# Kernel tuning notes

Measured on AMD Instinct MI355X. Metric: run time of the kernel, lower is better.

## Reference

```python
import jax, jax.numpy as jnp
import numpy as np

N = 50000   # nodes
E = 600000  # edges (avg degree ~12)
R = 8       # num_relations = 2 * n_speakers**2, n_speakers=2
B = 32      # num_bases = args.batch_size
GD, H1, H2 = 128, 128, 128


def setup_inputs() -> dict:
    key = jax.random.key(0)
    ks = jax.random.split(key, 16)
    w = lambda k, shape: jax.random.normal(k, shape, jnp.float32) * 0.05
    return {
        "node_features": jax.random.normal(ks[0], (N, GD), jnp.float32),
        "edge_index": jax.random.randint(ks[1], (2, E), 0, N),
        "edge_norm": jax.random.uniform(ks[2], (E,), jnp.float32),
        "edge_type": jax.random.randint(ks[3], (E,), 0, R),
        "basis": w(ks[4], (B, GD, H1)),
        "comp": w(ks[5], (R, B)),
        "root": w(ks[6], (GD, H1)),
        "bias1": jnp.zeros((H1,), jnp.float32),
        "w_key": w(ks[7], (H1, H2)),
        "b_key": jnp.zeros((H2,), jnp.float32),
        "w_query": w(ks[8], (H1, H2)),
        "b_query": jnp.zeros((H2,), jnp.float32),
        "w_value": w(ks[9], (H1, H2)),
        "b_value": jnp.zeros((H2,), jnp.float32),
        "w_skip": w(ks[10], (H1, H2)),
        "b_skip": jnp.zeros((H2,), jnp.float32),
    }


def reference(node_features, edge_index, edge_norm, edge_type, basis, comp,
              root, bias1, w_key, b_key, w_query, b_query, w_value, b_value,
              w_skip, b_skip):
    n = node_features.shape[0]
    r = comp.shape[0]
    src, dst = edge_index[0], edge_index[1]

    # ---- RGCNConv (basis decomposition, per-relation mean aggregation) ----
    W = jnp.einsum('rb,bio->rio', comp, basis)            # [R, GD, H1]
    xW = jnp.einsum('ni,rio->rno', node_features, W)      # [R, N, H1]
    msg = xW[edge_type, src]                              # [E, H1]
    seg = edge_type * n + dst                             # combined (relation, dst) segment id
    agg = jax.ops.segment_sum(msg, seg, num_segments=r * n).reshape(r, n, -1)
    cnt = jax.ops.segment_sum(jnp.ones(msg.shape[0], jnp.float32), seg,
                              num_segments=r * n).reshape(r, n, 1)
    h = (agg / jnp.maximum(cnt, 1.0)).sum(0) + node_features @ root + bias1

    # ---- ResGatedGraphConv: sigmoid(k_i + q_j) * v_j, sum-aggregated + skip ----
    k = h @ w_key + b_key
    q = h @ w_query + b_query
    v = h @ w_value + b_value
    m = jax.nn.sigmoid(k[dst] + q[src]) * v[src]          # [E, H2]
    out = jax.ops.segment_sum(m, dst, num_segments=n) + h @ w_skip + b_skip
    return out
```

## Files before the change

### kernel.cpp

```cpp
#include <hip/hip_runtime.h>
#include <stdint.h>

#define GD 128
#define H1 128
#define H2 128
#define NBASES 32
#define NREL 8
#define K1 (NREL*GD + GD)

typedef __attribute__((ext_vector_type(8))) short bf16x8;
typedef __attribute__((ext_vector_type(4))) float f32x4;

static inline size_t align256(size_t x){ return (x + 255) & ~(size_t)255; }

__device__ __forceinline__ float bf2f(uint32_t u16){
  union { uint32_t u; float f; } c; c.u = (u16 & 0xffffu) << 16; return c.f;
}
__device__ __forceinline__ unsigned short f2bf(float f){
  union { float f; uint32_t u; } c; c.f = f;
  uint32_t u = c.u;
  u += 0x7fffu + ((u >> 16) & 1u);
  return (unsigned short)(u >> 16);
}
__device__ __forceinline__ uint32_t pkbf(float a, float b){
  union { float f; uint32_t u; } ca, cb; ca.f = a; cb.f = b;
  return __builtin_amdgcn_perm(cb.u + 0x8000u, ca.u + 0x8000u, 0x07060302u);
}

__device__ __forceinline__ void async_copy16(void* lds_dst, const void* gsrc){
  __builtin_amdgcn_global_load_lds(
      (const __attribute__((address_space(1))) uint32_t*)gsrc,
      (__attribute__((address_space(3))) uint32_t*)lds_dst, 16, 0, 0);
}

__global__ void k_prep(const float* __restrict__ comp, const float* __restrict__ basis,
                       const float* __restrict__ root, unsigned short* __restrict__ B1t,
                       const float* __restrict__ wk, const float* __restrict__ wq,
                       const float* __restrict__ wv, const float* __restrict__ wsk,
                       const float* __restrict__ bk, const float* __restrict__ bq,
                       const float* __restrict__ bv, const float* __restrict__ bs,
                       unsigned short* __restrict__ B2t, float* __restrict__ Bb,
                       const float4* __restrict__ x, uint2* __restrict__ xout, int cnt4,
                       int4* __restrict__ cntz, int nz4){
  int b = blockIdx.x, t = threadIdx.x;
  if (b < 576){
    int idx = b*256 + t;
    int nn = idx / K1, kk = idx % K1;
    float v;
    if (kk < NREL*GD){
      int r = kk >> 7, i = kk & 127;
      float acc = 0.f;
      #pragma unroll
      for (int bb = 0; bb < NBASES; ++bb)
        acc += comp[r*NBASES + bb] * basis[((size_t)bb*GD + i)*H1 + nn];
      v = acc;
    } else {
      v = root[(size_t)(kk - NREL*GD)*H1 + nn];
    }
    B1t[idx] = f2bf(v);
  } else if (b < 576 + 256){
    int idx = (b - 576)*256 + t;
    int c = idx / H1, k = idx % H1;
    const float* w = (c < 128) ? wk : (c < 256) ? wq : (c < 384) ? wv : wsk;
    B2t[idx] = f2bf(w[(size_t)k*H2 + (c & 127)]);
    if (idx < 512){
      const float* bia = (idx < 128) ? bk : (idx < 256) ? bq : (idx < 384) ? bv : bs;
      Bb[idx] = bia[idx & 127];
    }
  } else {
    int cb = b - (576 + 256);
    int ncastb = (cnt4 + 255) >> 8;
    if (cb < ncastb){
      int i = cb*256 + t;
      if (i < cnt4){
        float4 v = x[i];
        uint2 o; o.x = pkbf(v.x, v.y); o.y = pkbf(v.z, v.w);
        xout[i] = o;
      }
    } else {
      int i = (cb - ncastb)*256 + t;
      if (i < nz4) cntz[i] = (int4){0,0,0,0};
    }
  }
}

__global__ void k_hist_rd(const int* __restrict__ dst, const int* __restrict__ typ,
                          int* __restrict__ cnt, int E, int n){
  int e = blockIdx.x*blockDim.x + threadIdx.x;
  if (e < E) atomicAdd(&cnt[typ[e]*n + dst[e]], 1);
}

__global__ void k_scanA(const int* __restrict__ deg, int* __restrict__ off,
                        int* __restrict__ btot, int len){
  __shared__ int wsum[16];
  int t = threadIdx.x, lane = t & 63, w = t >> 6;
  int i0 = blockIdx.x*8192 + t*8;
  int v[8];
  if (i0 + 7 < len){
    int4 va = *(const int4*)(deg + i0);
    int4 vb = *(const int4*)(deg + i0 + 4);
    v[0]=va.x; v[1]=va.y; v[2]=va.z; v[3]=va.w;
    v[4]=vb.x; v[5]=vb.y; v[6]=vb.z; v[7]=vb.w;
  } else {
    #pragma unroll
    for (int u = 0; u < 8; ++u) v[u] = (i0+u < len) ? deg[i0+u] : 0;
  }
  int s[8]; s[0] = v[0];
  #pragma unroll
  for (int u = 1; u < 8; ++u) s[u] = s[u-1] + v[u];
  int x = s[7];
  #pragma unroll
  for (int d = 1; d < 64; d <<= 1){
    int u = __shfl_up(x, d, 64);
    if (lane >= d) x += u;
  }
  if (lane == 63) wsum[w] = x;
  __syncthreads();
  if (t < 16){
    int y = wsum[t];
    #pragma unroll
    for (int d = 1; d < 16; d <<= 1){
      int u = __shfl_up(y, d, 16);
      if (t >= d) y += u;
    }
    wsum[t] = y;
  }
  __syncthreads();
  int woff = (w > 0) ? wsum[w-1] : 0;
  int excl = woff + x - s[7];
  #pragma unroll
  for (int u = 0; u < 8; ++u)
    if (i0+u < len) off[i0+u] = excl + s[u] - v[u];
  if (t == 0) btot[blockIdx.x] = wsum[15];
}

__global__ void k_scanB(const int* __restrict__ btot, int* __restrict__ off,
                        int* __restrict__ cursor, int len, int sentinel){
  int t = threadIdx.x, bid = blockIdx.x;
  int add = 0;
  for (int j = 0; j < bid; ++j) add += btot[j];
  int i0 = bid*8192 + t*8;
  #pragma unroll
  for (int u = 0; u < 8; ++u){
    int i = i0 + u;
    if (i < len){ int val = off[i] + add; off[i] = val; cursor[i] = val; }
  }
  if (bid == 0 && t == 0) off[len] = sentinel;
}

__global__ void k_scatter_rd(const int* __restrict__ src, const int* __restrict__ dst,
                             const int* __restrict__ typ, int* __restrict__ cursor,
                             int* __restrict__ pk, int E, int n){
  int e = blockIdx.x*blockDim.x + threadIdx.x;
  if (e >= E) return;
  int pos = atomicAdd(&cursor[typ[e]*n + dst[e]], 1);
  pk[pos] = src[e];
}

__global__ void k_edge1(const int* __restrict__ off_rd, const int* __restrict__ pk_rd,
                        const unsigned short* __restrict__ xbf,
                        unsigned short* __restrict__ Abig, int n, int npad){
  int wid = blockIdx.x*(blockDim.x >> 6) + (threadIdx.x >> 6);
  int lane = threadIdx.x & 63;
  if (wid >= npad) return;
  uint32_t* Arow = (uint32_t*)(Abig + (size_t)wid*K1);
  if (wid >= n){
    #pragma unroll
    for (int r = 0; r < 9; ++r) __builtin_nontemporal_store(0u, Arow + r*64 + lane);
    return;
  }
  const uint32_t* x32 = (const uint32_t*)xbf;
  int r8 = lane & 7;
  int o_r = off_rd[(size_t)r8*n + wid];
  int e_r = off_rd[(size_t)r8*n + wid + 1];
  int c_r = e_r - o_r;
  int c0_ = __builtin_amdgcn_readlane(c_r, 0), c1_ = __builtin_amdgcn_readlane(c_r, 1);
  int c2_ = __builtin_amdgcn_readlane(c_r, 2), c3_ = __builtin_amdgcn_readlane(c_r, 3);
  int c4_ = __builtin_amdgcn_readlane(c_r, 4), c5_ = __builtin_amdgcn_readlane(c_r, 5);
  int c6_ = __builtin_amdgcn_readlane(c_r, 6), c7_ = __builtin_amdgcn_readlane(c_r, 7);
  int o0_ = __builtin_amdgcn_readlane(o_r, 0), o1_ = __builtin_amdgcn_readlane(o_r, 1);
  int o2_ = __builtin_amdgcn_readlane(o_r, 2), o3_ = __builtin_amdgcn_readlane(o_r, 3);
  int o4_ = __builtin_amdgcn_readlane(o_r, 4), o5_ = __builtin_amdgcn_readlane(o_r, 5);
  int o6_ = __builtin_amdgcn_readlane(o_r, 6), o7_ = __builtin_amdgcn_readlane(o_r, 7);
  int p1 = c0_, p2 = p1 + c1_, p3 = p2 + c2_, p4 = p3 + c3_;
  int p5 = p4 + c4_, p6 = p5 + c5_, p7 = p6 + c6_, dg = p7 + c7_;

  float a0[8], a1[8];
  #pragma unroll
  for (int r = 0; r < 8; ++r){ a0[r] = 0.f; a1[r] = 0.f; }

  for (int jb = 0; jb < dg; jb += 64){
    int i = jb + lane;
    int adj = o0_, rel = 0;
    adj = (i >= p1) ? (o1_ - p1) : adj;  rel += (i >= p1);
    adj = (i >= p2) ? (o2_ - p2) : adj;  rel += (i >= p2);
    adj = (i >= p3) ? (o3_ - p3) : adj;  rel += (i >= p3);
    adj = (i >= p4) ? (o4_ - p4) : adj;  rel += (i >= p4);
    adj = (i >= p5) ? (o5_ - p5) : adj;  rel += (i >= p5);
    adj = (i >= p6) ? (o6_ - p6) : adj;  rel += (i >= p6);
    adj = (i >= p7) ? (o7_ - p7) : adj;  rel += (i >= p7);
    int m = dg - jb; if (m > 64) m = 64;
    int pj = (lane < m) ? pk_rd[adj + i] : 0;
    int jj = 0;
    for (; jj + 8 <= m; jj += 8){
      uint32_t g[8]; int rr[8];
      #pragma unroll
      for (int k = 0; k < 8; ++k){
        int s = __builtin_amdgcn_readlane(pj, jj + k);
        rr[k] = __builtin_amdgcn_readlane(rel, jj + k);
        g[k] = x32[(size_t)s*64 + lane];
      }
      #pragma unroll
      for (int k = 0; k < 8; ++k){
        float x0 = bf2f(g[k]), x1 = bf2f(g[k] >> 16);
        switch (rr[k]){
          case 0: a0[0]+=x0; a1[0]+=x1; break;
          case 1: a0[1]+=x0; a1[1]+=x1; break;
          case 2: a0[2]+=x0; a1[2]+=x1; break;
          case 3: a0[3]+=x0; a1[3]+=x1; break;
          case 4: a0[4]+=x0; a1[4]+=x1; break;
          case 5: a0[5]+=x0; a1[5]+=x1; break;
          case 6: a0[6]+=x0; a1[6]+=x1; break;
          default: a0[7]+=x0; a1[7]+=x1; break;
        }
      }
    }
    for (; jj < m; ++jj){
      int s = __builtin_amdgcn_readlane(pj, jj);
      int rk = __builtin_amdgcn_readlane(rel, jj);
      uint32_t gg = x32[(size_t)s*64 + lane];
      float x0 = bf2f(gg), x1 = bf2f(gg >> 16);
      switch (rk){
        case 0: a0[0]+=x0; a1[0]+=x1; break;
        case 1: a0[1]+=x0; a1[1]+=x1; break;
        case 2: a0[2]+=x0; a1[2]+=x1; break;
        case 3: a0[3]+=x0; a1[3]+=x1; break;
        case 4: a0[4]+=x0; a1[4]+=x1; break;
        case 5: a0[5]+=x0; a1[5]+=x1; break;
        case 6: a0[6]+=x0; a1[6]+=x1; break;
        default: a0[7]+=x0; a1[7]+=x1; break;
      }
    }
  }
  int cc[8] = {c0_, c1_, c2_, c3_, c4_, c5_, c6_, c7_};
  #pragma unroll
  for (int r = 0; r < 8; ++r){
    float inv = (cc[r] > 0) ? 1.f/(float)cc[r] : 0.f;
    __builtin_nontemporal_store(pkbf(a0[r]*inv, a1[r]*inv), Arow + r*64 + lane);
  }
  __builtin_nontemporal_store(x32[(size_t)wid*64 + lane], Arow + 512 + lane);
}

__launch_bounds__(256)
__global__ void k_gemm1(const unsigned short* __restrict__ A, const unsigned short* __restrict__ Bt,
                        const float* __restrict__ bias, unsigned short* __restrict__ h){
  __shared__ char lds[16384];
  int t = threadIdx.x, lane = t & 63, wave = t >> 6;
  int row0 = blockIdx.x * 128;
  int mrow = lane & 15, quad = lane >> 4;
  int wrow = (wave & 1) * 64, wcol = (wave >> 1) * 64;
  int s = (mrow >> 1) & 3;

  const unsigned short* Asrc = A + (size_t)(row0 + (t >> 2))*K1 + (((t & 3) ^ ((t >> 3) & 3)) << 3);
  const unsigned short* Bsrc = Bt + (size_t)(t >> 2)*K1 + (((t & 3) ^ ((t >> 3) & 3)) << 3);
  char* ldsw = lds + wave*1024;

  int aoff = (wrow + mrow)*64 + ((quad ^ s) << 4);
  int boff = 8192 + (wcol + mrow)*64 + ((quad ^ s) << 4);

  f32x4 acc[4][4];
  #pragma unroll
  for (int i = 0; i < 4; ++i)
    #pragma unroll
    for (int j = 0; j < 4; ++j) acc[i][j] = (f32x4){0.f,0.f,0.f,0.f};

  for (int kt = 0; kt < K1; kt += 32){
    __syncthreads();
    async_copy16(ldsw,         Asrc + kt);
    async_copy16(ldsw + 4096,  Asrc + (size_t)64*K1 + kt);
    async_copy16(ldsw + 8192,  Bsrc + kt);
    async_copy16(ldsw + 12288, Bsrc + (size_t)64*K1 + kt);
    __syncthreads();
    bf16x8 af[4], bf[4];
    #pragma unroll
    for (int i = 0; i < 4; ++i) af[i] = *(const bf16x8*)(lds + aoff + i*1024);
    #pragma unroll
    for (int j = 0; j < 4; ++j) bf[j] = *(const bf16x8*)(lds + boff + j*1024);
    #pragma unroll
    for (int i = 0; i < 4; ++i)
      #pragma unroll
      for (int j = 0; j < 4; ++j)
        acc[i][j] = __builtin_amdgcn_mfma_f32_16x16x32_bf16(af[i], bf[j], acc[i][j], 0, 0, 0);
  }
  #pragma unroll
  for (int j = 0; j < 4; ++j){
    int col = wcol + j*16 + mrow;
    float bcol = bias[col];
    #pragma unroll
    for (int i = 0; i < 4; ++i)
      #pragma unroll
      for (int rg = 0; rg < 4; ++rg){
        int row = wrow + i*16 + quad*4 + rg;
        h[(size_t)(row0 + row)*H1 + col] = f2bf(acc[i][j][rg] + bcol);
      }
  }
}

__launch_bounds__(256)
__global__ void k_gemm2(const unsigned short* __restrict__ A, const unsigned short* __restrict__ Bt,
                        const float* __restrict__ Bb, unsigned short* __restrict__ kqv,
                        unsigned short* __restrict__ skipb, int n){
  __shared__ char lds[16384];
  int t = threadIdx.x, lane = t & 63, wave = t >> 6;
  int row0 = blockIdx.x * 128;
  int c0 = blockIdx.y * 128;
  int mrow = lane & 15, quad = lane >> 4;
  int wrow = (wave & 1) * 64, wcol = (wave >> 1) * 64;
  int s = (mrow >> 1) & 3;

  const unsigned short* Asrc = A + (size_t)(row0 + (t >> 2))*H1 + (((t & 3) ^ ((t >> 3) & 3)) << 3);
  const unsigned short* Bsrc = Bt + (size_t)(c0 + (t >> 2))*H1 + (((t & 3) ^ ((t >> 3) & 3)) << 3);
  char* ldsw = lds + wave*1024;

  int aoff = (wrow + mrow)*64 + ((quad ^ s) << 4);
  int boff = 8192 + (wcol + mrow)*64 + ((quad ^ s) << 4);

  f32x4 acc[4][4];
  #pragma unroll
  for (int i = 0; i < 4; ++i)
    #pragma unroll
    for (int j = 0; j < 4; ++j) acc[i][j] = (f32x4){0.f,0.f,0.f,0.f};

  #pragma unroll
  for (int kt = 0; kt < H1; kt += 32){
    __syncthreads();
    async_copy16(ldsw,         Asrc + kt);
    async_copy16(ldsw + 4096,  Asrc + (size_t)64*H1 + kt);
    async_copy16(ldsw + 8192,  Bsrc + kt);
    async_copy16(ldsw + 12288, Bsrc + (size_t)64*H1 + kt);
    __syncthreads();
    bf16x8 af[4], bf[4];
    #pragma unroll
    for (int i = 0; i < 4; ++i) af[i] = *(const bf16x8*)(lds + aoff + i*1024);
    #pragma unroll
    for (int j = 0; j < 4; ++j) bf[j] = *(const bf16x8*)(lds + boff + j*1024);
    #pragma unroll
    for (int i = 0; i < 4; ++i)
      #pragma unroll
      for (int j = 0; j < 4; ++j)
        acc[i][j] = __builtin_amdgcn_mfma_f32_16x16x32_bf16(af[i], bf[j], acc[i][j], 0, 0, 0);
  }
  #pragma unroll
  for (int j = 0; j < 4; ++j){
    int col = c0 + wcol + j*16 + mrow;
    float bcol = Bb[col];
    #pragma unroll
    for (int i = 0; i < 4; ++i)
      #pragma unroll
// ... 14 lines not shown
        }
      }
  }
}

__global__ void k_edge2(const int* __restrict__ off_rd, const int* __restrict__ pk_rd,
                        const unsigned short* __restrict__ kqv,
                        const unsigned short* __restrict__ skipb,
                        float* __restrict__ out, int n){
  int wid = blockIdx.x*(blockDim.x >> 6) + (threadIdx.x >> 6);
  int lane = threadIdx.x & 63;
  if (wid >= n) return;
  const uint32_t* kv32 = (const uint32_t*)kqv;
  int r = lane & 7;
  int o_r = off_rd[(size_t)r*n + wid];
  int e_r = off_rd[(size_t)r*n + wid + 1];
  int c_r = e_r - o_r;
  int c0_ = __builtin_amdgcn_readlane(c_r, 0), c1_ = __builtin_amdgcn_readlane(c_r, 1);
  int c2_ = __builtin_amdgcn_readlane(c_r, 2), c3_ = __builtin_amdgcn_readlane(c_r, 3);
  int c4_ = __builtin_amdgcn_readlane(c_r, 4), c5_ = __builtin_amdgcn_readlane(c_r, 5);
  int c6_ = __builtin_amdgcn_readlane(c_r, 6), c7_ = __builtin_amdgcn_readlane(c_r, 7);
  int o0_ = __builtin_amdgcn_readlane(o_r, 0), o1_ = __builtin_amdgcn_readlane(o_r, 1);
  int o2_ = __builtin_amdgcn_readlane(o_r, 2), o3_ = __builtin_amdgcn_readlane(o_r, 3);
  int o4_ = __builtin_amdgcn_readlane(o_r, 4), o5_ = __builtin_amdgcn_readlane(o_r, 5);
  int o6_ = __builtin_amdgcn_readlane(o_r, 6), o7_ = __builtin_amdgcn_readlane(o_r, 7);
  int p1 = c0_, p2 = p1 + c1_, p3 = p2 + c2_, p4 = p3 + c3_;
  int p5 = p4 + c4_, p6 = p5 + c5_, p7 = p6 + c6_, dg = p7 + c7_;

  uint32_t ku = kv32[(size_t)wid*192 + lane];
  float k0 = bf2f(ku), k1 = bf2f(ku >> 16);
  float a0 = 0.f, a1 = 0.f;
  for (int jb = 0; jb < dg; jb += 64){
    int i = jb + lane;
    int adj = o0_;
    adj = (i >= p1) ? (o1_ - p1) : adj;
    adj = (i >= p2) ? (o2_ - p2) : adj;
    adj = (i >= p3) ? (o3_ - p3) : adj;
    adj = (i >= p4) ? (o4_ - p4) : adj;
    adj = (i >= p5) ? (o5_ - p5) : adj;
    adj = (i >= p6) ? (o6_ - p6) : adj;
    adj = (i >= p7) ? (o7_ - p7) : adj;
    int m = dg - jb; if (m > 64) m = 64;
    int pj = (lane < m) ? pk_rd[adj + i] : 0;
    int jj = 0;
    for (; jj + 8 <= m; jj += 8){
      uint2 q[8];
      #pragma unroll
      for (int k = 0; k < 8; ++k){
        int s = __builtin_amdgcn_readlane(pj, jj + k);
        q[k] = *(const uint2*)(kv32 + (size_t)s*192 + 64 + lane*2);
      }
      #pragma unroll
      for (int k = 0; k < 8; ++k){
        float qq0 = bf2f(q[k].x), qq1 = bf2f(q[k].x >> 16);
        float vv0 = bf2f(q[k].y), vv1 = bf2f(q[k].y >> 16);
        float g0 = 1.f / (1.f + __expf(-(k0 + qq0)));
        float g1 = 1.f / (1.f + __expf(-(k1 + qq1)));
        a0 += g0*vv0; a1 += g1*vv1;
      }
    }
    for (; jj < m; ++jj){
      int s = __builtin_amdgcn_readlane(pj, jj);
      uint2 qc = *(const uint2*)(kv32 + (size_t)s*192 + 64 + lane*2);
      float qq0 = bf2f(qc.x), qq1 = bf2f(qc.x >> 16);
      float vv0 = bf2f(qc.y), vv1 = bf2f(qc.y >> 16);
      float g0 = 1.f / (1.f + __expf(-(k0 + qq0)));
      float g1 = 1.f / (1.f + __expf(-(k1 + qq1)));
      a0 += g0*vv0; a1 += g1*vv1;
    }
  }
  uint32_t sk = ((const uint32_t*)skipb)[(size_t)wid*64 + lane];
  float2 cur; cur.x = a0 + bf2f(sk); cur.y = a1 + bf2f(sk >> 16);
  ((float2*)(out + (size_t)wid*H2))[lane] = cur;
}

extern "C" void kernel_launch(void* const* d_in, const int* in_sizes, int n_in,
                              void* d_out, int out_size, void* d_ws, size_t ws_size,
                              hipStream_t stream){
  const float* x     = (const float*)d_in[0];
  const int*   eidx  = (const int*)  d_in[1];
  const int*   etype = (const int*)  d_in[3];
  const float* basis = (const float*)d_in[4];
  const float* comp  = (const float*)d_in[5];
  const float* root  = (const float*)d_in[6];
  const float* bias1 = (const float*)d_in[7];
  const float* wk    = (const float*)d_in[8];
  const float* bk    = (const float*)d_in[9];
  const float* wq    = (const float*)d_in[10];
  const float* bq    = (const float*)d_in[11];
  const float* wv    = (const float*)d_in[12];
  const float* bv    = (const float*)d_in[13];
  const float* wsk   = (const float*)d_in[14];
  const float* bs    = (const float*)d_in[15];
  const int n = in_sizes[0] / GD;
  const int E = in_sizes[3];
  const int npad = (n + 127) & ~127;
  const int* esrc = eidx;
  const int* edst = eidx + E;
  float* out = (float*)d_out;

  char* w = (char*)d_ws;
  size_t off = 0;
  unsigned short* xbf  = (unsigned short*)(w + off); off = align256(off + (size_t)n*GD*2);
  unsigned short* Abig = (unsigned short*)(w + off); off = align256(off + (size_t)npad*K1*2);
  unsigned short* B1t  = (unsigned short*)(w + off); off = align256(off + (size_t)H1*K1*2);
  unsigned short* B2t  = (unsigned short*)(w + off); off = align256(off + (size_t)512*H1*2);
  float* Bb            = (float*)(w + off);          off = align256(off + 512*4);
  unsigned short* hbuf = (unsigned short*)(w + off); off = align256(off + (size_t)npad*H1*2);
  unsigned short* kqv  = (unsigned short*)(w + off); off = align256(off + (size_t)n*384*2);
  unsigned short* skipb= (unsigned short*)(w + off); off = align256(off + (size_t)npad*H2*2);
  int* cnt_rd          = (int*)(w + off);            off = align256(off + (size_t)(8*n+4)*4);
  int* off_rd          = (int*)(w + off);            off = align256(off + (size_t)(8*n+1)*4);
  int* cur_rd          = (int*)(w + off);            off = align256(off + (size_t)8*n*4);
  int* btot_rd         = (int*)(w + off);            off = align256(off + 64*4);
  int* pk_rd           = (int*)(w + off);            off = align256(off + (size_t)E*4);

  const int nblk_rd = (8*n + 8191) / 8192;
  const int cnt4 = n*GD/4;
  const int nz4  = (8*n + 3)/4;
  const int ncastb = (cnt4 + 255)/256;
  const int nzerob = (nz4 + 255)/256;

  k_prep<<<576 + 256 + ncastb + nzerob, 256, 0, stream>>>(
      comp, basis, root, B1t, wk, wq, wv, wsk, bk, bq, bv, bs, B2t, Bb,
      (const float4*)x, (uint2*)xbf, cnt4, (int4*)cnt_rd, nz4);
  k_hist_rd<<<(E + 255)/256, 256, 0, stream>>>(edst, etype, cnt_rd, E, n);
  k_scanA<<<nblk_rd, 1024, 0, stream>>>(cnt_rd, off_rd, btot_rd, 8*n);
  k_scanB<<<nblk_rd, 1024, 0, stream>>>(btot_rd, off_rd, cur_rd, 8*n, E);
  k_scatter_rd<<<(E + 255)/256, 256, 0, stream>>>(esrc, edst, etype, cur_rd, pk_rd, E, n);
  k_edge1<<<(npad + 3)/4, 256, 0, stream>>>(off_rd, pk_rd, xbf, Abig, n, npad);
  k_gemm1<<<npad/128, 256, 0, stream>>>(Abig, B1t, bias1, hbuf);
  k_gemm2<<<dim3(npad/128, 4), 256, 0, stream>>>(hbuf, B2t, Bb, kqv, skipb, n);
  k_edge2<<<(n + 3)/4, 256, 0, stream>>>(off_rd, pk_rd, kqv, skipb, out, n);
}
```

Measured before the change: 390.8 us.

## Transform per-relation features before aggregation and fuse bias and root into the edge gather

Reorders the relational conv. Each node's features are first multiplied by all eight relation weights plus root in one GEMM, giving a wide Z buffer. Edge aggregation then gathers rows of Z with per-edge 1/count weights and adds root and bias, so the large concatenated A matrix and its K=1152 GEMM go away. The histogram is also folded into the prep kernel and the count buffer is cleared with a memset. The cost of this is that the gather now reads slices of a much larger buffer (about 115MB) instead of the compact bf16 features, which may hurt cache locality.

Measured after the change: 380.6 us. 1.03x faster.

```diff
diff --git a/kernel.cpp b/kernel.cpp
--- a/kernel.cpp
+++ b/kernel.cpp
@@ -6,7 +6,7 @@
 #define H2 128
 #define NBASES 32
 #define NREL 8
-#define K1 (NREL*GD + GD)
+#define KZ 1152
 
 typedef __attribute__((ext_vector_type(8))) short bf16x8;
 typedef __attribute__((ext_vector_type(4))) float f32x4;
@@ -34,30 +34,32 @@
 }
 
 __global__ void k_prep(const float* __restrict__ comp, const float* __restrict__ basis,
-                       const float* __restrict__ root, unsigned short* __restrict__ B1t,
+                       const float* __restrict__ root, unsigned short* __restrict__ Bz,
                        const float* __restrict__ wk, const float* __restrict__ wq,
                        const float* __restrict__ wv, const float* __restrict__ wsk,
                        const float* __restrict__ bk, const float* __restrict__ bq,
                        const float* __restrict__ bv, const float* __restrict__ bs,
                        unsigned short* __restrict__ B2t, float* __restrict__ Bb,
                        const float4* __restrict__ x, uint2* __restrict__ xout, int cnt4,
-                       int4* __restrict__ cntz, int nz4){
+                       uint32_t* __restrict__ xpadz, int npadz,
+                       const int* __restrict__ edst, const int* __restrict__ etyp,
+                       int* __restrict__ cnt, int E, int n){
   int b = blockIdx.x, t = threadIdx.x;
   if (b < 576){
     int idx = b*256 + t;
-    int nn = idx / K1, kk = idx % K1;
+    int row = idx >> 7, i = idx & 127;
+    int r = row >> 7, o = row & 127;
     float v;
-    if (kk < NREL*GD){
-      int r = kk >> 7, i = kk & 127;
+    if (r < 8){
       float acc = 0.f;
       #pragma unroll
       for (int bb = 0; bb < NBASES; ++bb)
-        acc += comp[r*NBASES + bb] * basis[((size_t)bb*GD + i)*H1 + nn];
+        acc += comp[r*NBASES + bb] * basis[((size_t)bb*GD + i)*H1 + o];
       v = acc;
     } else {
-      v = root[(size_t)(kk - NREL*GD)*H1 + nn];
-    }
-    B1t[idx] = f2bf(v);
+      v = root[(size_t)i*H1 + o];
+    }
+    Bz[idx] = f2bf(v);
   } else if (b < 576 + 256){
     int idx = (b - 576)*256 + t;
     int c = idx / H1, k = idx % H1;
@@ -77,17 +79,14 @@
         uint2 o; o.x = pkbf(v.x, v.y); o.y = pkbf(v.z, v.w);
         xout[i] = o;
       }
+    } else if (cb < ncastb + 12){
+      int i = (cb - ncastb)*256 + t;
+      if (i < npadz) xpadz[i] = 0u;
     } else {
-      int i = (cb - ncastb)*256 + t;
-      if (i < nz4) cntz[i] = (int4){0,0,0,0};
-    }
-  }
-}
-
-__global__ void k_hist_rd(const int* __restrict__ dst, const int* __restrict__ typ,
-                          int* __restrict__ cnt, int E, int n){
-  int e = blockIdx.x*blockDim.x + threadIdx.x;
-  if (e < E) atomicAdd(&cnt[typ[e]*n + dst[e]], 1);
+      int e = (cb - ncastb - 12)*256 + t;
+      if (e < E) atomicAdd(&cnt[etyp[e]*n + edst[e]], 1);
+    }
+  }
 }
 
 __global__ void k_scanA(const int* __restrict__ deg, int* __restrict__ off,
@@ -157,23 +156,77 @@
   pk[pos] = src[e];
 }
 
+__launch_bounds__(256)
+__global__ void k_zgemm(const unsigned short* __restrict__ A, const unsigned short* __restrict__ Bt,
+                        unsigned short* __restrict__ Z){
+  __shared__ char lds[16384];
+  int t = threadIdx.x, lane = t & 63, wave = t >> 6;
+  int row0 = blockIdx.x * 128;
+  int c0 = blockIdx.y * 128;
+  int mrow = lane & 15, quad = lane >> 4;
+  int wrow = (wave & 1) * 64, wcol = (wave >> 1) * 64;
+  int s = (mrow >> 1) & 3;
+
+  const unsigned short* Asrc = A + (size_t)(row0 + (t >> 2))*H1 + (((t & 3) ^ ((t >> 3) & 3)) << 3);
+  const unsigned short* Bsrc = Bt + (size_t)(c0 + (t >> 2))*H1 + (((t & 3) ^ ((t >> 3) & 3)) << 3);
+  char* ldsw = lds + wave*1024;
+
+  int aoff = (wrow + mrow)*64 + ((quad ^ s) << 4);
+  int boff = 8192 + (wcol + mrow)*64 + ((quad ^ s) << 4);
+
+  f32x4 acc[4][4];
+  #pragma unroll
+  for (int i = 0; i < 4; ++i)
+    #pragma unroll
+    for (int j = 0; j < 4; ++j) acc[i][j] = (f32x4){0.f,0.f,0.f,0.f};
+
+  #pragma unroll
+  for (int kt = 0; kt < H1; kt += 32){
+    __syncthreads();
+    async_copy16(ldsw,         Asrc + kt);
+    async_copy16(ldsw + 4096,  Asrc + (size_t)64*H1 + kt);
+    async_copy16(ldsw + 8192,  Bsrc + kt);
+    async_copy16(ldsw + 12288, Bsrc + (size_t)64*H1 + kt);
+    __syncthreads();
+    bf16x8 af[4], bf[4];
+    #pragma unroll
+    for (int i = 0; i < 4; ++i) af[i] = *(const bf16x8*)(lds + aoff + i*1024);
+    #pragma unroll
+    for (int j = 0; j < 4; ++j) bf[j] = *(const bf16x8*)(lds + boff + j*1024);
+    #pragma unroll
+    for (int i = 0; i < 4; ++i)
+      #pragma unroll
+      for (int j = 0; j < 4; ++j)
+        acc[i][j] = __builtin_amdgcn_mfma_f32_16x16x32_bf16(af[i], bf[j], acc[i][j], 0, 0, 0);
+  }
+  #pragma unroll
+  for (int j = 0; j < 4; ++j){
+    int col = c0 + wcol + j*16 + mrow;
+    #pragma unroll
+    for (int i = 0; i < 4; ++i)
+      #pragma unroll
+      for (int rg = 0; rg < 4; ++rg){
+        int row = row0 + wrow + i*16 + quad*4 + rg;
+        Z[(size_t)row*KZ + col] = f2bf(acc[i][j][rg]);
+      }
+  }
+}
+
 __global__ void k_edge1(const int* __restrict__ off_rd, const int* __restrict__ pk_rd,
-                        const unsigned short* __restrict__ xbf,
-                        unsigned short* __restrict__ Abig, int n, int npad){
+                        const unsigned short* __restrict__ Zb,
+                        const float* __restrict__ bias1,
+                        unsigned short* __restrict__ h, int n, int npad){
   int wid = blockIdx.x*(blockDim.x >> 6) + (threadIdx.x >> 6);
   int lane = threadIdx.x & 63;
   if (wid >= npad) return;
-  uint32_t* Arow = (uint32_t*)(Abig + (size_t)wid*K1);
-  if (wid >= n){
-    #pragma unroll
-    for (int r = 0; r < 9; ++r) __builtin_nontemporal_store(0u, Arow + r*64 + lane);
-    return;
-  }
-  const uint32_t* x32 = (const uint32_t*)xbf;
+  uint32_t* hrow = (uint32_t*)(h + (size_t)wid*H1);
+  if (wid >= n){ hrow[lane] = 0u; return; }
+  const uint32_t* Z32 = (const uint32_t*)Zb;
   int r8 = lane & 7;
   int o_r = off_rd[(size_t)r8*n + wid];
   int e_r = off_rd[(size_t)r8*n + wid + 1];
   int c_r = e_r - o_r;
+  float ic_r = (c_r > 0) ? (1.f/(float)c_r) : 0.f;
   int c0_ = __builtin_amdgcn_readlane(c_r, 0), c1_ = __builtin_amdgcn_readlane(c_r, 1);
   int c2_ = __builtin_amdgcn_readlane(c_r, 2), c3_ = __builtin_amdgcn_readlane(c_r, 3);
   int c4_ = __builtin_amdgcn_readlane(c_r, 4), c5_ = __builtin_amdgcn_readlane(c_r, 5);
@@ -182,128 +235,58 @@
   int o2_ = __builtin_amdgcn_readlane(o_r, 2), o3_ = __builtin_amdgcn_readlane(o_r, 3);
   int o4_ = __builtin_amdgcn_readlane(o_r, 4), o5_ = __builtin_amdgcn_readlane(o_r, 5);
   int o6_ = __builtin_amdgcn_readlane(o_r, 6), o7_ = __builtin_amdgcn_readlane(o_r, 7);
+  float i0f = __int_as_float(__builtin_amdgcn_readlane(__float_as_int(ic_r), 0));
+  float i1f = __int_as_float(__builtin_amdgcn_readlane(__float_as_int(ic_r), 1));
+  float i2f = __int_as_float(__builtin_amdgcn_readlane(__float_as_int(ic_r), 2));
+  float i3f = __int_as_float(__builtin_amdgcn_readlane(__float_as_int(ic_r), 3));
+  float i4f = __int_as_float(__builtin_amdgcn_readlane(__float_as_int(ic_r), 4));
+  float i5f = __int_as_float(__builtin_amdgcn_readlane(__float_as_int(ic_r), 5));
+  float i6f = __int_as_float(__builtin_amdgcn_readlane(__float_as_int(ic_r), 6));
+  float i7f = __int_as_float(__builtin_amdgcn_readlane(__float_as_int(ic_r), 7));
   int p1 = c0_, p2 = p1 + c1_, p3 = p2 + c2_, p4 = p3 + c3_;
   int p5 = p4 + c4_, p6 = p5 + c5_, p7 = p6 + c6_, dg = p7 + c7_;
 
-  float a0[8], a1[8];
-  #pragma unroll
-  for (int r = 0; r < 8; ++r){ a0[r] = 0.f; a1[r] = 0.f; }
-
+  float a0 = 0.f, a1 = 0.f;
   for (int jb = 0; jb < dg; jb += 64){
     int i = jb + lane;
     int adj = o0_, rel = 0;
-    adj = (i >= p1) ? (o1_ - p1) : adj;  rel += (i >= p1);
-    adj = (i >= p2) ? (o2_ - p2) : adj;  rel += (i >= p2);
-    adj = (i >= p3) ? (o3_ - p3) : adj;  rel += (i >= p3);
-    adj = (i >= p4) ? (o4_ - p4) : adj;  rel += (i >= p4);
-    adj = (i >= p5) ? (o5_ - p5) : adj;  rel += (i >= p5);
-    adj = (i >= p6) ? (o6_ - p6) : adj;  rel += (i >= p6);
-    adj = (i >= p7) ? (o7_ - p7) : adj;  rel += (i >= p7);
+    float wv = i0f;
+    adj = (i >= p1) ? (o1_ - p1) : adj;  rel += (i >= p1);  wv = (i >= p1) ? i1f : wv;
+    adj = (i >= p2) ? (o2_ - p2) : adj;  rel += (i >= p2);  wv = (i >= p2) ? i2f : wv;
+    adj = (i >= p3) ? (o3_ - p3) : adj;  rel += (i >= p3);  wv = (i >= p3) ? i3f : wv;
+    adj = (i >= p4) ? (o4_ - p4) : adj;  rel += (i >= p4);  wv = (i >= p4) ? i4f : wv;
+    adj = (i >= p5) ? (o5_ - p5) : adj;  rel += (i >= p5);  wv = (i >= p5) ? i5f : wv;
+    adj = (i >= p6) ? (o6_ - p6) : adj;  rel += (i >= p6);  wv = (i >= p6) ? i6f : wv;
+    adj = (i >= p7) ? (o7_ - p7) : adj;  rel += (i >= p7);  wv = (i >= p7) ? i7f : wv;
     int m = dg - jb; if (m > 64) m = 64;
     int pj = (lane < m) ? pk_rd[adj + i] : 0;
+    int gidx = pj*(KZ/2) + rel*64;
     int jj = 0;
     for (; jj + 8 <= m; jj += 8){
-      uint32_t g[8]; int rr[8];
+      uint32_t g[8]; float wgt[8];
       #pragma unroll
       for (int k = 0; k < 8; ++k){
-        int s = __builtin_amdgcn_readlane(pj, jj + k);
-        rr[k] = __builtin_amdgcn_readlane(rel, jj + k);
-        g[k] = x32[(size_t)s*64 + lane];
+        int gx = __builtin_amdgcn_readlane(gidx, jj + k);
+        wgt[k] = __int_as_float(__builtin_amdgcn_readlane(__float_as_int(wv), jj + k));
+        g[k] = Z32[(size_t)(uint32_t)gx + lane];
       }
       #pragma unroll
       for (int k = 0; k < 8; ++k){
-        float x0 = bf2f(g[k]), x1 = bf2f(g[k] >> 16);
-        switch (rr[k]){
-          case 0: a0[0]+=x0; a1[0]+=x1; break;
-          case 1: a0[1]+=x0; a1[1]+=x1; break;
-          case 2: a0[2]+=x0; a1[2]+=x1; break;
-          case 3: a0[3]+=x0; a1[3]+=x1; break;
-          case 4: a0[4]+=x0; a1[4]+=x1; break;
-          case 5: a0[5]+=x0; a1[5]+=x1; break;
-          case 6: a0[6]+=x0; a1[6]+=x1; break;
-          default: a0[7]+=x0; a1[7]+=x1; break;
-        }
+        a0 += bf2f(g[k]) * wgt[k];
+        a1 += bf2f(g[k] >> 16) * wgt[k];
       }
     }
     for (; jj < m; ++jj){
-      int s = __builtin_amdgcn_readlane(pj, jj);
-      int rk = __builtin_amdgcn_readlane(rel, jj);
-      uint32_t gg = x32[(size_t)s*64 + lane];
-      float x0 = bf2f(gg), x1 = bf2f(gg >> 16);
-      switch (rk){
-        case 0: a0[0]+=x0; a1[0]+=x1; break;
-        case 1: a0[1]+=x0; a1[1]+=x1; break;
-        case 2: a0[2]+=x0; a1[2]+=x1; break;
-        case 3: a0[3]+=x0; a1[3]+=x1; break;
-        case 4: a0[4]+=x0; a1[4]+=x1; break;
-        case 5: a0[5]+=x0; a1[5]+=x1; break;
-        case 6: a0[6]+=x0; a1[6]+=x1; break;
-        default: a0[7]+=x0; a1[7]+=x1; break;
-      }
-    }
-  }
-  int cc[8] = {c0_, c1_, c2_, c3_, c4_, c5_, c6_, c7_};
-  #pragma unroll
-  for (int r = 0; r < 8; ++r){
-    float inv = (cc[r] > 0) ? 1.f/(float)cc[r] : 0.f;
-    __builtin_nontemporal_store(pkbf(a0[r]*inv, a1[r]*inv), Arow + r*64 + lane);
-  }
-  __builtin_nontemporal_store(x32[(size_t)wid*64 + lane], Arow + 512 + lane);
-}
-
-__launch_bounds__(256)
-__global__ void k_gemm1(const unsigned short* __restrict__ A, const unsigned short* __restrict__ Bt,
-                        const float* __restrict__ bias, unsigned short* __restrict__ h){
-  __shared__ char lds[16384];
-  int t = threadIdx.x, lane = t & 63, wave = t >> 6;
-  int row0 = blockIdx.x * 128;
-  int mrow = lane & 15, quad = lane >> 4;
-  int wrow = (wave & 1) * 64, wcol = (wave >> 1) * 64;
-  int s = (mrow >> 1) & 3;
-
-  const unsigned short* Asrc = A + (size_t)(row0 + (t >> 2))*K1 + (((t & 3) ^ ((t >> 3) & 3)) << 3);
-  const unsigned short* Bsrc = Bt + (size_t)(t >> 2)*K1 + (((t & 3) ^ ((t >> 3) & 3)) << 3);
-  char* ldsw = lds + wave*1024;
-
-  int aoff = (wrow + mrow)*64 + ((quad ^ s) << 4);
-  int boff = 8192 + (wcol + mrow)*64 + ((quad ^ s) << 4);
-
-  f32x4 acc[4][4];
-  #pragma unroll
-  for (int i = 0; i < 4; ++i)
-    #pragma unroll
-    for (int j = 0; j < 4; ++j) acc[i][j] = (f32x4){0.f,0.f,0.f,0.f};
-
-  for (int kt = 0; kt < K1; kt += 32){
-    __syncthreads();
-    async_copy16(ldsw,         Asrc + kt);
-    async_copy16(ldsw + 4096,  Asrc + (size_t)64*K1 + kt);
-    async_copy16(ldsw + 8192,  Bsrc + kt);
-    async_copy16(ldsw + 12288, Bsrc + (size_t)64*K1 + kt);
-    __syncthreads();
-    bf16x8 af[4], bf[4];
-    #pragma unroll
-    for (int i = 0; i < 4; ++i) af[i] = *(const bf16x8*)(lds + aoff + i*1024);
-    #pragma unroll
-    for (int j = 0; j < 4; ++j) bf[j] = *(const bf16x8*)(lds + boff + j*1024);
-    #pragma unroll
-    for (int i = 0; i < 4; ++i)
-      #pragma unroll
-      for (int j = 0; j < 4; ++j)
-        acc[i][j] = __builtin_amdgcn_mfma_f32_16x16x32_bf16(af[i], bf[j], acc[i][j], 0, 0, 0);
-  }
-  #pragma unroll
-  for (int j = 0; j < 4; ++j){
-    int col = wcol + j*16 + mrow;
-    float bcol = bias[col];
-    #pragma unroll
-    for (int i = 0; i < 4; ++i)
-      #pragma unroll
-      for (int rg = 0; rg < 4; ++rg){
-        int row = wrow + i*16 + quad*4 + rg;
-        h[(size_t)(row0 + row)*H1 + col] = f2bf(acc[i][j][rg] + bcol);
-      }
-  }
+      int gx = __builtin_amdgcn_readlane(gidx, jj);
+      float wg = __int_as_float(__builtin_amdgcn_readlane(__float_as_int(wv), jj));
+      uint32_t gg = Z32[(size_t)(uint32_t)gx + lane];
+      a0 += bf2f(gg) * wg;
+      a1 += bf2f(gg >> 16) * wg;
+    }
+  }
+  uint32_t zr = Z32[(size_t)wid*(KZ/2) + 512 + lane];
+  float2 bb = ((const float2*)bias1)[lane];
+  hrow[lane] = pkbf(a0 + bf2f(zr) + bb.x, a1 + bf2f(zr >> 16) + bb.y);
 }
 
 __launch_bounds__(256)
@@ -473,9 +456,9 @@
 
   char* w = (char*)d_ws;
   size_t off = 0;
-  unsigned short* xbf  = (unsigned short*)(w + off); off = align256(off + (size_t)n*GD*2);
-  unsigned short* Abig = (unsigned short*)(w + off); off = align256(off + (size_t)npad*K1*2);
-  unsigned short* B1t  = (unsigned short*)(w + off); off = align256(off + (size_t)H1*K1*2);
+  unsigned short* xbf  = (unsigned short*)(w + off); off = align256(off + (size_t)npad*GD*2);
+  unsigned short* Zbuf = (unsigned short*)(w + off); off = align256(off + (size_t)npad*KZ*2);
+  unsigned short* Bz   = (unsigned short*)(w + off); off = align256(off + (size_t)KZ*H1*2);
   unsigned short* B2t  = (unsigned short*)(w + off); off = align256(off + (size_t)512*H1*2);
   float* Bb            = (float*)(w + off);          off = align256(off + 512*4);
   unsigned short* hbuf = (unsigned short*)(w + off); off = align256(off + (size_t)npad*H1*2);
@@ -489,19 +472,22 @@
 
   const int nblk_rd = (8*n + 8191) / 8192;
   const int cnt4 = n*GD/4;
-  const int nz4  = (8*n + 3)/4;
   const int ncastb = (cnt4 + 255)/256;
-  const int nzerob = (nz4 + 255)/256;
-
-  k_prep<<<576 + 256 + ncastb + nzerob, 256, 0, stream>>>(
-      comp, basis, root, B1t, wk, wq, wv, wsk, bk, bq, bv, bs, B2t, Bb,
-      (const float4*)x, (uint2*)xbf, cnt4, (int4*)cnt_rd, nz4);
-  k_hist_rd<<<(E + 255)/256, 256, 0, stream>>>(edst, etype, cnt_rd, E, n);
+  const int histb  = (E + 255)/256;
+  const int npadz  = (npad - n)*GD/2;
+
+  hipMemsetAsync(cnt_rd, 0, (size_t)8*n*4, stream);
+
+  k_prep<<<576 + 256 + ncastb + 12 + histb, 256, 0, stream>>>(
+      comp, basis, root, Bz, wk, wq, wv, wsk, bk, bq, bv, bs, B2t, Bb,
+      (const float4*)x, (uint2*)xbf, cnt4,
+      (uint32_t*)(xbf + (size_t)n*GD), npadz,
+      edst, etype, cnt_rd, E, n);
   k_scanA<<<nblk_rd, 1024, 0, stream>>>(cnt_rd, off_rd, btot_rd, 8*n);
   k_scanB<<<nblk_rd, 1024, 0, stream>>>(btot_rd, off_rd, cur_rd, 8*n, E);
   k_scatter_rd<<<(E + 255)/256, 256, 0, stream>>>(esrc, edst, etype, cur_rd, pk_rd, E, n);
-  k_edge1<<<(npad + 3)/4, 256, 0, stream>>>(off_rd, pk_rd, xbf, Abig, n, npad);
-  k_gemm1<<<npad/128, 256, 0, stream>>>(Abig, B1t, bias1, hbuf);
+  k_zgemm<<<dim3(npad/128, KZ/128), 256, 0, stream>>>(xbf, Bz, Zbuf);
+  k_edge1<<<(npad + 3)/4, 256, 0, stream>>>(off_rd, pk_rd, Zbuf, bias1, hbuf, n, npad);
   k_gemm2<<<dim3(npad/128, 4), 256, 0, stream>>>(hbuf, B2t, Bb, kqv, skipb, n);
   k_edge2<<<(n + 3)/4, 256, 0, stream>>>(off_rd, pk_rd, kqv, skipb, out, n);
 }
```

## Fuse relation aggregation with first GEMM via LDS tile, merge histogram into prep

Applied to the files above, without the earlier changes.

Replaces the edge1 gather kernel and the separate gemm1 with a single kernel that aggregates 32 nodes' per-relation means into a shared-memory A tile and multiplies it by the weight matrix with MFMA. This removes the round trip through the large Abig intermediate in global memory. The histogram atomics are folded into the prep kernel, with the counter zeroing done by a memset. A 4-edge unrolled tail is also added to both edge loops. The trade-off is that each block now holds about 74KB of LDS and reads B1t straight from global, which lowers occupancy. There is also an ordering risk: the histogram atomics run in the same launch as prep, so they depend on the memset finishing first.

New measurement: 403.2 us. 3.2% more time.

```diff
diff --git a/kernel.cpp b/kernel.cpp
--- a/kernel.cpp
+++ b/kernel.cpp
@@ -7,6 +7,7 @@
 #define NBASES 32
 #define NREL 8
 #define K1 (NREL*GD + GD)
+#define AROW 580
 
 typedef __attribute__((ext_vector_type(8))) short bf16x8;
 typedef __attribute__((ext_vector_type(4))) float f32x4;
@@ -25,12 +26,6 @@
 __device__ __forceinline__ uint32_t pkbf(float a, float b){
   union { float f; uint32_t u; } ca, cb; ca.f = a; cb.f = b;
   return __builtin_amdgcn_perm(cb.u + 0x8000u, ca.u + 0x8000u, 0x07060302u);
-}
-
-__device__ __forceinline__ void async_copy16(void* lds_dst, const void* gsrc){
-  __builtin_amdgcn_global_load_lds(
-      (const __attribute__((address_space(1))) uint32_t*)gsrc,
-      (__attribute__((address_space(3))) uint32_t*)lds_dst, 16, 0, 0);
 }
 
 __global__ void k_prep(const float* __restrict__ comp, const float* __restrict__ basis,
@@ -41,7 +36,8 @@
                        const float* __restrict__ bv, const float* __restrict__ bs,
                        unsigned short* __restrict__ B2t, float* __restrict__ Bb,
                        const float4* __restrict__ x, uint2* __restrict__ xout, int cnt4,
-                       int4* __restrict__ cntz, int nz4){
+                       const int* __restrict__ edst, const int* __restrict__ etyp,
+                       int* __restrict__ cnt, int E, int n){
   int b = blockIdx.x, t = threadIdx.x;
   if (b < 576){
     int idx = b*256 + t;
@@ -78,16 +74,10 @@
         xout[i] = o;
       }
     } else {
-      int i = (cb - ncastb)*256 + t;
-      if (i < nz4) cntz[i] = (int4){0,0,0,0};
-    }
-  }
-}
-
-__global__ void k_hist_rd(const int* __restrict__ dst, const int* __restrict__ typ,
-                          int* __restrict__ cnt, int E, int n){
-  int e = blockIdx.x*blockDim.x + threadIdx.x;
-  if (e < E) atomicAdd(&cnt[typ[e]*n + dst[e]], 1);
+      int e = (cb - ncastb)*256 + t;
+      if (e < E) atomicAdd(&cnt[etyp[e]*n + edst[e]], 1);
+    }
+  }
 }
 
 __global__ void k_scanA(const int* __restrict__ deg, int* __restrict__ off,
@@ -157,63 +147,110 @@
   pk[pos] = src[e];
 }
 
-__global__ void k_edge1(const int* __restrict__ off_rd, const int* __restrict__ pk_rd,
-                        const unsigned short* __restrict__ xbf,
-                        unsigned short* __restrict__ Abig, int n, int npad){
-  int wid = blockIdx.x*(blockDim.x >> 6) + (threadIdx.x >> 6);
-  int lane = threadIdx.x & 63;
-  if (wid >= npad) return;
-  uint32_t* Arow = (uint32_t*)(Abig + (size_t)wid*K1);
-  if (wid >= n){
-    #pragma unroll
-    for (int r = 0; r < 9; ++r) __builtin_nontemporal_store(0u, Arow + r*64 + lane);
-    return;
-  }
+__launch_bounds__(512)
+__global__ void k_fused1(const int* __restrict__ off_rd, const int* __restrict__ pk_rd,
+                         const unsigned short* __restrict__ xbf,
+                         const unsigned short* __restrict__ B1t,
+                         const float* __restrict__ bias1,
+                         unsigned short* __restrict__ h, int n){
+  __shared__ uint32_t Atile[32*AROW];
   const uint32_t* x32 = (const uint32_t*)xbf;
-  int r8 = lane & 7;
-  int o_r = off_rd[(size_t)r8*n + wid];
-  int e_r = off_rd[(size_t)r8*n + wid + 1];
-  int c_r = e_r - o_r;
-  int c0_ = __builtin_amdgcn_readlane(c_r, 0), c1_ = __builtin_amdgcn_readlane(c_r, 1);
-  int c2_ = __builtin_amdgcn_readlane(c_r, 2), c3_ = __builtin_amdgcn_readlane(c_r, 3);
-  int c4_ = __builtin_amdgcn_readlane(c_r, 4), c5_ = __builtin_amdgcn_readlane(c_r, 5);
-  int c6_ = __builtin_amdgcn_readlane(c_r, 6), c7_ = __builtin_amdgcn_readlane(c_r, 7);
-  int o0_ = __builtin_amdgcn_readlane(o_r, 0), o1_ = __builtin_amdgcn_readlane(o_r, 1);
-  int o2_ = __builtin_amdgcn_readlane(o_r, 2), o3_ = __builtin_amdgcn_readlane(o_r, 3);
-  int o4_ = __builtin_amdgcn_readlane(o_r, 4), o5_ = __builtin_amdgcn_readlane(o_r, 5);
-  int o6_ = __builtin_amdgcn_readlane(o_r, 6), o7_ = __builtin_amdgcn_readlane(o_r, 7);
-  int p1 = c0_, p2 = p1 + c1_, p3 = p2 + c2_, p4 = p3 + c3_;
-  int p5 = p4 + c4_, p6 = p5 + c5_, p7 = p6 + c6_, dg = p7 + c7_;
-
-  float a0[8], a1[8];
-  #pragma unroll
-  for (int r = 0; r < 8; ++r){ a0[r] = 0.f; a1[r] = 0.f; }
-
-  for (int jb = 0; jb < dg; jb += 64){
-    int i = jb + lane;
-    int adj = o0_, rel = 0;
-    adj = (i >= p1) ? (o1_ - p1) : adj;  rel += (i >= p1);
-    adj = (i >= p2) ? (o2_ - p2) : adj;  rel += (i >= p2);
-    adj = (i >= p3) ? (o3_ - p3) : adj;  rel += (i >= p3);
-    adj = (i >= p4) ? (o4_ - p4) : adj;  rel += (i >= p4);
-    adj = (i >= p5) ? (o5_ - p5) : adj;  rel += (i >= p5);
-    adj = (i >= p6) ? (o6_ - p6) : adj;  rel += (i >= p6);
-    adj = (i >= p7) ? (o7_ - p7) : adj;  rel += (i >= p7);
-    int m = dg - jb; if (m > 64) m = 64;
-    int pj = (lane < m) ? pk_rd[adj + i] : 0;
-    int jj = 0;
-    for (; jj + 8 <= m; jj += 8){
-      uint32_t g[8]; int rr[8];
-      #pragma unroll
-      for (int k = 0; k < 8; ++k){
-        int s = __builtin_amdgcn_readlane(pj, jj + k);
-        rr[k] = __builtin_amdgcn_readlane(rel, jj + k);
-        g[k] = x32[(size_t)s*64 + lane];
-      }
-      #pragma unroll
-      for (int k = 0; k < 8; ++k){
-        float x0 = bf2f(g[k]), x1 = bf2f(g[k] >> 16);
-        switch (rr[k]){
+  int t = threadIdx.x, lane = t & 63, wave = t >> 6;
+  int node_base = blockIdx.x * 32;
+
+  for (int i = 0; i < 4; ++i){
+    int m = wave*4 + i;
+    int nd = node_base + m;
+    uint32_t* Arow = Atile + m*AROW;
+    if (nd >= n){
+      #pragma unroll
+      for (int r = 0; r < 9; ++r) Arow[r*64 + lane] = 0u;
+      continue;
+    }
+    int r8 = lane & 7;
+    int o_r = off_rd[(size_t)r8*n + nd];
+    int e_r = off_rd[(size_t)r8*n + nd + 1];
+    int c_r = e_r - o_r;
+    int c0_ = __builtin_amdgcn_readlane(c_r, 0), c1_ = __builtin_amdgcn_readlane(c_r, 1);
+    int c2_ = __builtin_amdgcn_readlane(c_r, 2), c3_ = __builtin_amdgcn_readlane(c_r, 3);
+    int c4_ = __builtin_amdgcn_readlane(c_r, 4), c5_ = __builtin_amdgcn_readlane(c_r, 5);
+    int c6_ = __builtin_amdgcn_readlane(c_r, 6), c7_ = __builtin_amdgcn_readlane(c_r, 7);
+    int o0_ = __builtin_amdgcn_readlane(o_r, 0), o1_ = __builtin_amdgcn_readlane(o_r, 1);
+    int o2_ = __builtin_amdgcn_readlane(o_r, 2), o3_ = __builtin_amdgcn_readlane(o_r, 3);
+    int o4_ = __builtin_amdgcn_readlane(o_r, 4), o5_ = __builtin_amdgcn_readlane(o_r, 5);
+    int o6_ = __builtin_amdgcn_readlane(o_r, 6), o7_ = __builtin_amdgcn_readlane(o_r, 7);
+    int p1 = c0_, p2 = p1 + c1_, p3 = p2 + c2_, p4 = p3 + c3_;
+    int p5 = p4 + c4_, p6 = p5 + c5_, p7 = p6 + c6_, dg = p7 + c7_;
+
+    float a0[8], a1[8];
+    #pragma unroll
+    for (int r = 0; r < 8; ++r){ a0[r] = 0.f; a1[r] = 0.f; }
+
+    for (int jb = 0; jb < dg; jb += 64){
+      int ii = jb + lane;
+      int adj = o0_, rel = 0;
+      adj = (ii >= p1) ? (o1_ - p1) : adj;  rel += (ii >= p1);
+      adj = (ii >= p2) ? (o2_ - p2) : adj;  rel += (ii >= p2);
+      adj = (ii >= p3) ? (o3_ - p3) : adj;  rel += (ii >= p3);
+      adj = (ii >= p4) ? (o4_ - p4) : adj;  rel += (ii >= p4);
+      adj = (ii >= p5) ? (o5_ - p5) : adj;  rel += (ii >= p5);
+      adj = (ii >= p6) ? (o6_ - p6) : adj;  rel += (ii >= p6);
+      adj = (ii >= p7) ? (o7_ - p7) : adj;  rel += (ii >= p7);
+      int mm = dg - jb; if (mm > 64) mm = 64;
+      int pj = (lane < mm) ? pk_rd[adj + ii] : 0;
+      int jj = 0;
+      for (; jj + 8 <= mm; jj += 8){
+        uint32_t g[8]; int rr[8];
+        #pragma unroll
+        for (int k = 0; k < 8; ++k){
+          int s = __builtin_amdgcn_readlane(pj, jj + k);
+          rr[k] = __builtin_amdgcn_readlane(rel, jj + k);
+          g[k] = x32[(size_t)s*64 + lane];
+        }
+        #pragma unroll
+        for (int k = 0; k < 8; ++k){
+          float x0 = bf2f(g[k]), x1 = bf2f(g[k] >> 16);
+          switch (rr[k]){
+            case 0: a0[0]+=x0; a1[0]+=x1; break;
+            case 1: a0[1]+=x0; a1[1]+=x1; break;
+            case 2: a0[2]+=x0; a1[2]+=x1; break;
+            case 3: a0[3]+=x0; a1[3]+=x1; break;
+            case 4: a0[4]+=x0; a1[4]+=x1; break;
+            case 5: a0[5]+=x0; a1[5]+=x1; break;
+            case 6: a0[6]+=x0; a1[6]+=x1; break;
+            default: a0[7]+=x0; a1[7]+=x1; break;
+          }
+        }
+      }
+      for (; jj + 4 <= mm; jj += 4){
+        uint32_t g[4]; int rr[4];
+        #pragma unroll
+        for (int k = 0; k < 4; ++k){
+          int s = __builtin_amdgcn_readlane(pj, jj + k);
+          rr[k] = __builtin_amdgcn_readlane(rel, jj + k);
+          g[k] = x32[(size_t)s*64 + lane];
+        }
+        #pragma unroll
+        for (int k = 0; k < 4; ++k){
+          float x0 = bf2f(g[k]), x1 = bf2f(g[k] >> 16);
+          switch (rr[k]){
+            case 0: a0[0]+=x0; a1[0]+=x1; break;
+            case 1: a0[1]+=x0; a1[1]+=x1; break;
+            case 2: a0[2]+=x0; a1[2]+=x1; break;
+            case 3: a0[3]+=x0; a1[3]+=x1; break;
+            case 4: a0[4]+=x0; a1[4]+=x1; break;
+            case 5: a0[5]+=x0; a1[5]+=x1; break;
+            case 6: a0[6]+=x0; a1[6]+=x1; break;
+            default: a0[7]+=x0; a1[7]+=x1; break;
+          }
+        }
+      }
+      for (; jj < mm; ++jj){
+        int s = __builtin_amdgcn_readlane(pj, jj);
+        int rk = __builtin_amdgcn_readlane(rel, jj);
+        uint32_t gg = x32[(size_t)s*64 + lane];
+        float x0 = bf2f(gg), x1 = bf2f(gg >> 16);
+        switch (rk){
           case 0: a0[0]+=x0; a1[0]+=x1; break;
           case 1: a0[1]+=x0; a1[1]+=x1; break;
           case 2: a0[2]+=x0; a1[2]+=x1; break;
@@ -225,85 +262,43 @@
         }
       }
     }
-    for (; jj < m; ++jj){
-      int s = __builtin_amdgcn_readlane(pj, jj);
-      int rk = __builtin_amdgcn_readlane(rel, jj);
-      uint32_t gg = x32[(size_t)s*64 + lane];
-      float x0 = bf2f(gg), x1 = bf2f(gg >> 16);
-      switch (rk){
-        case 0: a0[0]+=x0; a1[0]+=x1; break;
-        case 1: a0[1]+=x0; a1[1]+=x1; break;
-        case 2: a0[2]+=x0; a1[2]+=x1; break;
-        case 3: a0[3]+=x0; a1[3]+=x1; break;
-        case 4: a0[4]+=x0; a1[4]+=x1; break;
-        case 5: a0[5]+=x0; a1[5]+=x1; break;
-        case 6: a0[6]+=x0; a1[6]+=x1; break;
-        default: a0[7]+=x0; a1[7]+=x1; break;
-      }
-    }
-  }
-  int cc[8] = {c0_, c1_, c2_, c3_, c4_, c5_, c6_, c7_};
-  #pragma unroll
-  for (int r = 0; r < 8; ++r){
-    float inv = (cc[r] > 0) ? 1.f/(float)cc[r] : 0.f;
-    __builtin_nontemporal_store(pkbf(a0[r]*inv, a1[r]*inv), Arow + r*64 + lane);
-  }
-  __builtin_nontemporal_store(x32[(size_t)wid*64 + lane], Arow + 512 + lane);
-}
-
-__launch_bounds__(256)
-__global__ void k_gemm1(const unsigned short* __restrict__ A, const unsigned short* __restrict__ Bt,
-                        const float* __restrict__ bias, unsigned short* __restrict__ h){
-  __shared__ char lds[16384];
-  int t = threadIdx.x, lane = t & 63, wave = t >> 6;
-  int row0 = blockIdx.x * 128;
+    int cc[8] = {c0_, c1_, c2_, c3_, c4_, c5_, c6_, c7_};
+    #pragma unroll
+    for (int r = 0; r < 8; ++r){
+      float inv = (cc[r] > 0) ? 1.f/(float)cc[r] : 0.f;
+      Arow[r*64 + lane] = pkbf(a0[r]*inv, a1[r]*inv);
+    }
+    Arow[512 + lane] = x32[(size_t)nd*64 + lane];
+  }
+  __syncthreads();
+
   int mrow = lane & 15, quad = lane >> 4;
-  int wrow = (wave & 1) * 64, wcol = (wave >> 1) * 64;
-  int s = (mrow >> 1) & 3;
-
-  const unsigned short* Asrc = A + (size_t)(row0 + (t >> 2))*K1 + (((t & 3) ^ ((t >> 3) & 3)) << 3);
-  const unsigned short* Bsrc = Bt + (size_t)(t >> 2)*K1 + (((t & 3) ^ ((t >> 3) & 3)) << 3);
-  char* ldsw = lds + wave*1024;
-
-  int aoff = (wrow + mrow)*64 + ((quad ^ s) << 4);
-  int boff = 8192 + (wcol + mrow)*64 + ((quad ^ s) << 4);
-
-  f32x4 acc[4][4];
-  #pragma unroll
-  for (int i = 0; i < 4; ++i)
-    #pragma unroll
-    for (int j = 0; j < 4; ++j) acc[i][j] = (f32x4){0.f,0.f,0.f,0.f};
-
-  for (int kt = 0; kt < K1; kt += 32){
-    __syncthreads();
-    async_copy16(ldsw,         Asrc + kt);
-    async_copy16(ldsw + 4096,  Asrc + (size_t)64*K1 + kt);
-    async_copy16(ldsw + 8192,  Bsrc + kt);
-    async_copy16(ldsw + 12288, Bsrc + (size_t)64*K1 + kt);
-    __syncthreads();
-    bf16x8 af[4], bf[4];
-    #pragma unroll
-    for (int i = 0; i < 4; ++i) af[i] = *(const bf16x8*)(lds + aoff + i*1024);
-    #pragma unroll
-    for (int j = 0; j < 4; ++j) bf[j] = *(const bf16x8*)(lds + boff + j*1024);
-    #pragma unroll
-    for (int i = 0; i < 4; ++i)
-      #pragma unroll
-      for (int j = 0; j < 4; ++j)
-        acc[i][j] = __builtin_amdgcn_mfma_f32_16x16x32_bf16(af[i], bf[j], acc[i][j], 0, 0, 0);
-  }
-  #pragma unroll
-  for (int j = 0; j < 4; ++j){
-    int col = wcol + j*16 + mrow;
-    float bcol = bias[col];
-    #pragma unroll
-    for (int i = 0; i < 4; ++i)
-      #pragma unroll
-      for (int rg = 0; rg < 4; ++rg){
-        int row = wrow + i*16 + quad*4 + rg;
-        h[(size_t)(row0 + row)*H1 + col] = f2bf(acc[i][j][rg] + bcol);
-      }
-  }
+  int nr = wave*16 + mrow;
+  const unsigned short* Bp = B1t + (size_t)nr*K1 + quad*8;
+  f32x4 acc0 = (f32x4){0.f,0.f,0.f,0.f};
+  f32x4 acc1 = (f32x4){0.f,0.f,0.f,0.f};
+  #pragma unroll
+  for (int c = 0; c < 36; ++c){
+    bf16x8 bfr = *(const bf16x8*)(Bp + c*32);
+    bf16x8 af0 = *(const bf16x8*)(Atile + mrow*AROW + c*16 + quad*4);
+    bf16x8 af1 = *(const bf16x8*)(Atile + (16 + mrow)*AROW + c*16 + quad*4);
+    acc0 = __builtin_amdgcn_mfma_f32_16x16x32_bf16(af0, bfr, acc0, 0, 0, 0);
+    acc1 = __builtin_amdgcn_mfma_f32_16x16x32_bf16(af1, bfr, acc1, 0, 0, 0);
+  }
+  float bcol = bias1[nr];
+  #pragma unroll
+  for (int rg = 0; rg < 4; ++rg){
+    int row0 = node_base + quad*4 + rg;
+    int row1 = node_base + 16 + quad*4 + rg;
+    h[(size_t)row0*H1 + nr] = f2bf(acc0[rg] + bcol);
+    h[(size_t)row1*H1 + nr] = f2bf(acc1[rg] + bcol);
+  }
+}
+
+__device__ __forceinline__ void async_copy16(void* lds_dst, const void* gsrc){
+  __builtin_amdgcn_global_load_lds(
+      (const __attribute__((address_space(1))) uint32_t*)gsrc,
+      (__attribute__((address_space(3))) uint32_t*)lds_dst, 16, 0, 0);
 }
 
 __launch_bounds__(256)
@@ -424,6 +419,22 @@
       }
       #pragma unroll
       for (int k = 0; k < 8; ++k){
+        float qq0 = bf2f(q[k].x), qq1 = bf2f(q[k].x >> 16);
+        float vv0 = bf2f(q[k].y), vv1 = bf2f(q[k].y >> 16);
+        float g0 = 1.f / (1.f + __expf(-(k0 + qq0)));
+        float g1 = 1.f / (1.f + __expf(-(k1 + qq1)));
+        a0 += g0*vv0; a1 += g1*vv1;
+      }
+    }
+    for (; jj + 4 <= m; jj += 4){
+      uint2 q[4];
+      #pragma unroll
+      for (int k = 0; k < 4; ++k){
+        int s = __builtin_amdgcn_readlane(pj, jj + k);
+        q[k] = *(const uint2*)(kv32 + (size_t)s*192 + 64 + lane*2);
+      }
+      #pragma unroll
+      for (int k = 0; k < 4; ++k){
         float qq0 = bf2f(q[k].x), qq1 = bf2f(q[k].x >> 16);
         float vv0 = bf2f(q[k].y), vv1 = bf2f(q[k].y >> 16);
         float g0 = 1.f / (1.f + __expf(-(k0 + qq0)));
@@ -474,7 +485,6 @@
   char* w = (char*)d_ws;
   size_t off = 0;
   unsigned short* xbf  = (unsigned short*)(w + off); off = align256(off + (size_t)n*GD*2);
-  unsigned short* Abig = (unsigned short*)(w + off); off = align256(off + (size_t)npad*K1*2);
   unsigned short* B1t  = (unsigned short*)(w + off); off = align256(off + (size_t)H1*K1*2);
   unsigned short* B2t  = (unsigned short*)(w + off); off = align256(off + (size_t)512*H1*2);
   float* Bb            = (float*)(w + off);          off = align256(off + 512*4);
@@ -489,19 +499,18 @@
 
   const int nblk_rd = (8*n + 8191) / 8192;
   const int cnt4 = n*GD/4;
-  const int nz4  = (8*n + 3)/4;
   const int ncastb = (cnt4 + 255)/256;
-  const int nzerob = (nz4 + 255)/256;
-
-  k_prep<<<576 + 256 + ncastb + nzerob, 256, 0, stream>>>(
+  const int histb  = (E + 255)/256;
+
+  hipMemsetAsync(cnt_rd, 0, (size_t)8*n*4, stream);
+
+  k_prep<<<576 + 256 + ncastb + histb, 256, 0, stream>>>(
       comp, basis, root, B1t, wk, wq, wv, wsk, bk, bq, bv, bs, B2t, Bb,
-      (const float4*)x, (uint2*)xbf, cnt4, (int4*)cnt_rd, nz4);
-  k_hist_rd<<<(E + 255)/256, 256, 0, stream>>>(edst, etype, cnt_rd, E, n);
+      (const float4*)x, (uint2*)xbf, cnt4, edst, etype, cnt_rd, E, n);
   k_scanA<<<nblk_rd, 1024, 0, stream>>>(cnt_rd, off_rd, btot_rd, 8*n);
   k_scanB<<<nblk_rd, 1024, 0, stream>>>(btot_rd, off_rd, cur_rd, 8*n, E);
   k_scatter_rd<<<(E + 255)/256, 256, 0, stream>>>(esrc, edst, etype, cur_rd, pk_rd, E, n);
-  k_edge1<<<(npad + 3)/4, 256, 0, stream>>>(off_rd, pk_rd, xbf, Abig, n, npad);
-  k_gemm1<<<npad/128, 256, 0, stream>>>(Abig, B1t, bias1, hbuf);
+  k_fused1<<<npad/32, 512, 0, stream>>>(off_rd, pk_rd, xbf, B1t, bias1, hbuf, n);
   k_gemm2<<<dim3(npad/128, 4), 256, 0, stream>>>(hbuf, B2t, Bb, kqv, skipb, n);
   k_edge2<<<(n + 3)/4, 256, 0, stream>>>(off_rd, pk_rd, kqv, skipb, out, n);
 }
```
